# Kernel optimization log

Hardware: AMD Instinct MI355X
Metric: run time of the kernel (lower is better)

The kernel has to match this reference:

```python
import jax, jax.numpy as jnp
import numpy as np

# Dimensions
B2, T, C = 400, 120, 128          # x: ((B*V), T, C)
V = 25                            # num_point (skeleton joints)
NH_A = 3                          # adjacency heads (A.shape[0])
HEADS, DH = 8, 64                 # attention heads, dim_head
INNER = HEADS * DH                # 512
QKV_C = INNER * 3                 # 1536 = GCN out_channels
EPS = 1e-5                        # torch BatchNorm2d default eps


def setup_inputs() -> dict:
    key = jax.random.key(0)
    ks = jax.random.split(key, 12)
    z = lambda *s: jnp.zeros(s, jnp.float32)
    o = lambda *s: jnp.ones(s, jnp.float32)
    return {
        "x": jax.random.normal(ks[0], (B2, T, C), jnp.float32),
        # GCN shared topology (num_head, V, V)
        "A": jax.random.normal(ks[1], (NH_A, V, V), jnp.float32) * 0.2,
        # per-head 1x1 conv weights/biases (stacked)
        "conv_w": jax.random.normal(ks[2], (NH_A, QKV_C, C), jnp.float32) * 0.02,
        "conv_b": jax.random.normal(ks[3], (NH_A, QKV_C), jnp.float32) * 0.01,
        # main BatchNorm2d (eval mode, running stats)
        "bn_gamma": jax.random.uniform(ks[4], (QKV_C,), jnp.float32, 0.5, 1.5),
        "bn_beta": z(QKV_C),
        "bn_mean": z(QKV_C),
        "bn_var": o(QKV_C),
        # down path: 1x1 conv + BatchNorm2d (in_c != out_c)
        "down_w": jax.random.normal(ks[5], (QKV_C, C), jnp.float32) * 0.02,
        "down_b": z(QKV_C),
        "dbn_gamma": jax.random.uniform(ks[6], (QKV_C,), jnp.float32, 0.5, 1.5),
        "dbn_beta": z(QKV_C),
        "dbn_mean": z(QKV_C),
        "dbn_var": o(QKV_C),
        # to_out Linear(inner_dim -> dim)
        "out_w": jax.random.normal(ks[7], (C, INNER), jnp.float32) * 0.02,
        "out_b": z(C),
    }


def _bn_eval(y, gamma, beta, mean, var):
    # y: (b, o, t, v); BN over channel axis 1, eval mode
    inv = gamma / jnp.sqrt(var + EPS)
    return y * inv[None, :, None, None] + (beta - mean * inv)[None, :, None, None]


def reference(x, A, conv_w, conv_b, bn_gamma, bn_beta, bn_mean, bn_var,
              down_w, down_b, dbn_gamma, dbn_beta, dbn_mean, dbn_var,
              out_w, out_b):
    B = B2 // V
    # '(b v) t c -> b c t v'
    x4 = x.reshape(B, V, T, C).transpose(0, 3, 2, 1)  # (b, c, t, v)

    # ---- GCN projection: sum_h Conv1x1_h(A_h @ x) ----
    z = jnp.einsum('hvu,bctu->bhctv', A, x4)                    # (b,h,c,t,v)
    y = jnp.einsum('hoc,bhctv->botv', conv_w, z)                # (b,O,t,v)
    y = y + conv_b.sum(0)[None, :, None, None]
    y = _bn_eval(y, bn_gamma, bn_beta, bn_mean, bn_var)

    d = jnp.einsum('oc,bctv->botv', down_w, x4) + down_b[None, :, None, None]
    d = _bn_eval(d, dbn_gamma, dbn_beta, dbn_mean, dbn_var)

    y = jax.nn.relu(y + d)                                      # (b,O,t,v)

    # ---- attention over time per (batch*joint) row ----
    qkv = y.transpose(0, 3, 2, 1).reshape(B2, T, QKV_C)         # '(b v) t c'
    q, k, v = jnp.split(qkv, 3, axis=-1)
    split_heads = lambda t: t.reshape(B2, T, HEADS, DH).transpose(0, 2, 1, 3)
    q, k, v = split_heads(q), split_heads(k), split_heads(v)

    dots = jnp.einsum('bhid,bhjd->bhij', q, k) * (DH ** -0.5)
    mask = jnp.tril(jnp.ones((T, T), bool))                     # causal mask
    dots = jnp.where(mask[None, None], dots, -jnp.inf)
    attn = jax.nn.softmax(dots, axis=-1)                        # (B2,H,T,T)

    o = jnp.einsum('bhij,bhjd->bhid', attn, v)
    o = o.transpose(0, 2, 1, 3).reshape(B2, T, INNER)
    out = o @ out_w.T + out_b                                   # (B2,T,C)
    return out, attn
```

## Files before the change

kernel.cpp:

```cpp
#include <hip/hip_runtime.h>


typedef __bf16 bf16;
typedef __bf16 bf16x8 __attribute__((ext_vector_type(8)));
typedef __bf16 bf16x4 __attribute__((ext_vector_type(4)));
typedef float  f32x4  __attribute__((ext_vector_type(4)));
typedef __attribute__((address_space(1))) const void* gptr1;
typedef __attribute__((address_space(3))) void*       lptr3;

#define GLL16(g, l) __builtin_amdgcn_global_load_lds((gptr1)(g), (lptr3)(l), 16, 0, 0)
#define MFMA16(a, b, c) __builtin_amdgcn_mfma_f32_16x16x32_bf16(a, b, c, 0, 0, 0)

__global__ __launch_bounds__(256) void build_weights(
    const float* __restrict__ conv_w, const float* __restrict__ conv_b,
    const float* __restrict__ g1, const float* __restrict__ be1,
    const float* __restrict__ mu1, const float* __restrict__ va1,
    const float* __restrict__ down_w, const float* __restrict__ down_b,
    const float* __restrict__ g2, const float* __restrict__ be2,
    const float* __restrict__ mu2, const float* __restrict__ va2,
    const float* __restrict__ out_w,
    bf16* __restrict__ wcat, bf16* __restrict__ wout, float* __restrict__ bias)
{
    int idx = blockIdx.x * 256 + threadIdx.x;
    if (idx < 1536 * 512) {
        int o = idx >> 9, k = idx & 511;
        float s, w;
        if (k < 384) {
            int h = k >> 7, c = k & 127;
            s = g1[o] * rsqrtf(va1[o] + 1e-5f);
            w = conv_w[(h * 1536 + o) * 128 + c];
        } else {
            s = g2[o] * rsqrtf(va2[o] + 1e-5f);
            w = down_w[o * 128 + (k - 384)];
        }
        wcat[idx] = (bf16)(w * s);
    }
    int i2 = idx - 1536 * 512;
    if (i2 >= 0 && i2 < 128 * 512) wout[i2] = (bf16)out_w[i2];
    int i3 = idx - (1536 * 512 + 128 * 512);
    if (i3 >= 0 && i3 < 1536) {
        int o = i3;
        float s1 = g1[o] * rsqrtf(va1[o] + 1e-5f);
        float s2 = g2[o] * rsqrtf(va2[o] + 1e-5f);
        float cb = conv_b[o] + conv_b[1536 + o] + conv_b[2 * 1536 + o];
        bias[o] = cb * s1 + be1[o] - mu1[o] * s1
                + down_b[o] * s2 + be2[o] - mu2[o] * s2;
    }
}

__global__ __launch_bounds__(256) void transform(
    const float* __restrict__ x, const float* __restrict__ A,
    bf16* __restrict__ zt)
{
    __shared__ float xs[25][128];
    const int tid = threadIdx.x;
    const int bt = blockIdx.x;
    const int b = bt / 120, t = bt - b * 120;
    for (int i = tid; i < 25 * 128; i += 256) {
        int u = i >> 7, c = i & 127;
        xs[u][c] = x[((size_t)(b * 25 + u) * 120 + t) * 128 + c];
    }
    __syncthreads();
    const int c = tid & 127, g = tid >> 7;
    float xr[25];
    #pragma unroll
    for (int u = 0; u < 25; u++) xr[u] = xs[u][c];
    for (int idx = g; idx < 75; idx += 2) {
        int h = idx / 25, v = idx - h * 25;
        const float* Ap = A + (h * 25 + v) * 25;
        float acc = 0.f;
        #pragma unroll
        for (int u = 0; u < 25; u++) acc += Ap[u] * xr[u];
        zt[((size_t)(b * 25 + v) * 120 + t) * 512 + h * 128 + c] = (bf16)acc;
    }
    for (int v = g; v < 25; v += 2)
        zt[((size_t)(b * 25 + v) * 120 + t) * 512 + 384 + c] = (bf16)xs[v][c];
}

__global__ __launch_bounds__(256) void gemm_qkv(
    const bf16* __restrict__ wcat, const bf16* __restrict__ zt,
    const float* __restrict__ bias,
    bf16* __restrict__ qg, bf16* __restrict__ kg, bf16* __restrict__ vtg)
{
    __shared__ __align__(16) char smem[49152];
    const int tid = threadIdx.x, lane = tid & 63, wv = tid >> 6;
    const int wrow = wv >> 1, wcol = wv & 1;
    const int NB = 4500, q8 = NB >> 3, r8 = NB & 7;
    const int xcd = blockIdx.x & 7, sidx = blockIdx.x >> 3;
    const int vid = (xcd < r8 ? xcd * (q8 + 1) : r8 * (q8 + 1) + (xcd - r8) * q8) + sidx;
    const int mt = vid % 12, nt = vid / 12;
    const int colb = lane & 15, rg = lane >> 4;

    f32x4 zz = {0.f, 0.f, 0.f, 0.f};
    f32x4 acc[4][4];
    #pragma unroll
    for (int i = 0; i < 4; i++)
        #pragma unroll
        for (int j = 0; j < 4; j++) acc[i][j] = zz;

    const char* gA = (const char*)wcat + (size_t)mt * 128 * 1024;
    const char* gB = (const char*)zt + (size_t)nt * 128 * 1024;
    const int srow = lane >> 2;
    const int skb = (((lane & 3) ^ ((lane >> 3) & 3)) * 16);
    const int rgs = rg ^ ((colb >> 1) & 3);
    const int aoff0 = (wrow * 64 + colb) * 64 + rgs * 16;
    const int boff0 = (wcol * 64 + colb) * 64 + rgs * 16;

    #define STAGE_QKV(kt, b) do {                                              \
        char* As_ = smem + (b) * 16384; char* Bs_ = As_ + 8192;                \
        _Pragma("unroll")                                                      \
        for (int j = 0; j < 2; j++) {                                          \
            int ck = wv * 2 + j;  int row = ck * 16 + srow;                    \
            GLL16(gA + (size_t)row * 1024 + (kt) * 64 + skb, As_ + ck * 1024); \
            GLL16(gB + (size_t)row * 1024 + (kt) * 64 + skb, Bs_ + ck * 1024); \
        } } while (0)

    STAGE_QKV(0, 0);
    STAGE_QKV(1, 1);
    asm volatile("s_waitcnt vmcnt(4)" ::: "memory");
    __builtin_amdgcn_s_barrier();
    for (int kt = 0; kt < 16; kt++) {
        const char* As = smem + (kt % 3) * 16384;
        const char* Bs = As + 8192;
        bf16x8 af[4], bfr[4];
        #pragma unroll
        for (int m = 0; m < 4; m++)
            af[m] = *(const bf16x8*)(As + aoff0 + m * 1024);
        #pragma unroll
        for (int n = 0; n < 4; n++)
            bfr[n] = *(const bf16x8*)(Bs + boff0 + n * 1024);
        int kn = kt + 2;
        STAGE_QKV(kn < 16 ? kn : 15, kn % 3);
        __builtin_amdgcn_s_setprio(1);
        #pragma unroll
        for (int m = 0; m < 4; m++)
            #pragma unroll
            for (int n = 0; n < 4; n++)
                acc[m][n] = MFMA16(af[m], bfr[n], acc[m][n]);
        __builtin_amdgcn_s_setprio(0);
        asm volatile("s_waitcnt vmcnt(4)" ::: "memory");
        __builtin_amdgcn_s_barrier();
    }
    __builtin_amdgcn_sched_barrier(0);

    const int mtb = mt * 128, ntb = nt * 128;
    const int which = mtb >> 9;

    if (which < 2) {
        bf16* Lt = (bf16*)smem;
        const float qs = (which == 0) ? 0.125f : 1.0f;
        #pragma unroll
        for (int m = 0; m < 4; m++) {
            int o0 = wrow * 64 + m * 16 + rg * 4;
            float b0 = bias[mtb + o0 + 0], b1 = bias[mtb + o0 + 1];
            float b2 = bias[mtb + o0 + 2], b3 = bias[mtb + o0 + 3];
            #pragma unroll
            for (int nn = 0; nn < 4; nn++) {
                int n_ = wcol * 64 + nn * 16 + colb;
                bf16x4 pk;
                pk[0] = (bf16)(fmaxf(acc[m][nn][0] + b0, 0.f) * qs);
                pk[1] = (bf16)(fmaxf(acc[m][nn][1] + b1, 0.f) * qs);
                pk[2] = (bf16)(fmaxf(acc[m][nn][2] + b2, 0.f) * qs);
                pk[3] = (bf16)(fmaxf(acc[m][nn][3] + b3, 0.f) * qs);
                *(bf16x4*)((char*)Lt + n_ * 256 + ((o0 * 2) ^ ((n_ & 7) << 4))) = pk;
            }
        }
        __syncthreads();
        bf16* dst = (which == 0) ? qg : kg;
        #pragma unroll
        for (int i = 0; i < 8; i++) {
            int ch = i * 256 + tid;
            int n_ = ch >> 4, c16 = ch & 15;
            int ng = ntb + n_;
            int grp = ng / 120, t = ng - grp * 120;
            int o = mtb + c16 * 8;
            int hd = (o >> 6) & 7, dd0 = o & 63;
            bf16x8 vv = *(const bf16x8*)((const char*)Lt + n_ * 256 +
                                         ((c16 * 16) ^ ((n_ & 7) << 4)));
            *(bf16x8*)(dst + ((size_t)(grp * 8 + hd) * 120 + t) * 64 + dd0) = vv;
        }
    } else {
        #pragma unroll
        for (int m = 0; m < 4; m++) {
            #pragma unroll
            for (int reg = 0; reg < 4; reg++) {
                int o = mtb + wrow * 64 + m * 16 + rg * 4 + reg;
                float bo = bias[o];
                int hd = (o >> 6) & 7, dd = o & 63;
                #pragma unroll
                for (int nn = 0; nn < 4; nn++) {
                    int n = ntb + wcol * 64 + nn * 16 + colb;
                    int grp = n / 120, t = n - grp * 120;
                    float val = fmaxf(acc[m][nn][reg] + bo, 0.f);
                    vtg[((size_t)(grp * 8 + hd) * 64 + dd) * 128 + t] = (bf16)val;
                }
            }
        }
    }
    #undef STAGE_QKV
}

__global__ __launch_bounds__(256) void attn_k(
    const bf16* __restrict__ qg, const bf16* __restrict__ kg,
    const bf16* __restrict__ vtg, float* __restrict__ attn_out,
    bf16* __restrict__ og)
{
    __shared__ __align__(16) char sm[49152];
    char* Vt = sm;
    char* Ks = sm + 16384;
    char* Ps = sm + 16384;
    const int tid = threadIdx.x, lane = tid & 63, wv = tid >> 6;
    const int bh = blockIdx.x;
    const int colb = lane & 15, rg = lane >> 4;

    const char* ksrc = (const char*)kg + (size_t)bh * 15360;
    const char* vsrc = (const char*)vtg + (size_t)bh * 16384;
    #pragma unroll
    for (int is = 0; is < 4; is++) {
        int cb = is * 256 + wv * 64;
        if (cb < 960) {
            int bb = (cb + lane) * 16;
            int row = bb >> 7;
            int gsrc = (bb & ~127) | ((bb & 127) ^ ((row & 7) << 4));
            GLL16(ksrc + gsrc, Ks + cb * 16);
        }
    }
    const char* qsrc = (const char*)qg + (size_t)bh * 15360;
    bf16x8 qf[2][2];
    #pragma unroll
    for (int kk = 0; kk < 2; kk++)
        #pragma unroll
        for (int m = 0; m < 2; m++) {
            int row = wv * 32 + m * 16 + colb;
            qf[kk][m] = *(const bf16x8*)(qsrc + (size_t)row * 128 + rg * 16 + kk * 64);
        }
    #pragma unroll
    for (int is = 0; is < 4; is++) {
        int cb = is * 256 + wv * 64;
        int bb = (cb + lane) * 16;
        int row = bb >> 8;
        int gsrc = (bb & ~255) | ((bb & 255) ^ ((row & 7) << 4));
        GLL16(vsrc + gsrc, Vt + cb * 16);
    }
    asm volatile("s_waitcnt vmcnt(4)" ::: "memory");
    __builtin_amdgcn_s_barrier();
    if (tid < 64) {
        f32x4 z = {0.f, 0.f, 0.f, 0.f};
        int r = 120 + (tid >> 3), off = (tid & 7) * 16;
        *(f32x4*)(Ks + r * 128 + off) = z;
    }
    asm volatile("s_waitcnt lgkmcnt(0)" ::: "memory");
    __builtin_amdgcn_s_barrier();

    f32x4 accs[2][8];
    #pragma unroll
    for (int m = 0; m < 2; m++)
        #pragma unroll
        for (int ct = 0; ct < 8; ct++) accs[m][ct] = (f32x4){0.f, 0.f, 0.f, 0.f};
    #pragma unroll
    for (int kk = 0; kk < 2; kk++) {
        #pragma unroll
        for (int ct = 0; ct < 8; ct++) {
            int rk = ct * 16 + colb;
            int byo = rk * 128 + ((rg * 16 + kk * 64) ^ ((rk & 7) << 4));
            bf16x8 bk = *(const bf16x8*)(Ks + byo);
            accs[0][ct] = MFMA16(qf[kk][0], bk, accs[0][ct]);
            accs[1][ct] = MFMA16(qf[kk][1], bk, accs[1][ct]);
        }
    }
    asm volatile("s_waitcnt vmcnt(0)" ::: "memory");
    __builtin_amdgcn_s_barrier();
    if (tid >= 64 && tid < 128) {
        int d = tid - 64;
        f32x4 z = {0.f, 0.f, 0.f, 0.f};
        *(f32x4*)(Vt + d * 256 + (240 ^ ((d & 7) << 4))) = z;
    }

    const int rqb = wv * 32;
    #pragma unroll
    for (int m = 0; m < 2; m++) {
        #pragma unroll
        for (int reg = 0; reg < 4; reg++) {
            int t_q = rqb + m * 16 + rg * 4 + reg;
            float s[8], mx = -1e30f;
            #pragma unroll
            for (int ct = 0; ct < 8; ct++) {
                int col = ct * 16 + colb;
                bool valid = (col <= t_q) && (col < 120);
                s[ct] = valid ? accs[m][ct][reg] : -1e30f;
                mx = fmaxf(mx, s[ct]);
            }
            #pragma unroll
            for (int d = 1; d < 16; d <<= 1) mx = fmaxf(mx, __shfl_xor(mx, d, 64));
            float p[8], sum = 0.f;
            #pragma unroll
            for (int ct = 0; ct < 8; ct++) {
                p[ct] = (s[ct] > -1e29f) ? __expf(s[ct] - mx) : 0.f;
                sum += p[ct];
            }
            #pragma unroll
            for (int d = 1; d < 16; d <<= 1) sum += __shfl_xor(sum, d, 64);
            float inv = 1.f / sum;
            #pragma unroll
            for (int ct = 0; ct < 8; ct++) {
                int col = ct * 16 + colb;
                int byo = t_q * 256 + ((col * 2) ^ ((t_q & 7) << 4));
                *(bf16*)(Ps + byo) = (bf16)(p[ct] * inv);
            }
        }
    }
    asm volatile("s_waitcnt lgkmcnt(0)" ::: "memory");
    __builtin_amdgcn_s_barrier();

    f32x4 acco[2][4];
    #pragma unroll
    for (int m = 0; m < 2; m++)
        #pragma unroll
        for (int dt = 0; dt < 4; dt++) acco[m][dt] = (f32x4){0.f, 0.f, 0.f, 0.f};
    for (int kk = 0; kk <= wv; kk++) {
        bf16x8 ap[2];
        #pragma unroll
        for (int m = 0; m < 2; m++) {
            int row = rqb + m * 16 + colb;
            int byo = row * 256 + ((rg * 16 + kk * 64) ^ ((row & 7) << 4));
            ap[m] = *(const bf16x8*)(Ps + byo);
        }
        #pragma unroll
        for (int dt = 0; dt < 4; dt++) {
            int rd = dt * 16 + colb;
            int byo = rd * 256 + ((rg * 16 + kk * 64) ^ ((rd & 7) << 4));
            bf16x8 bv = *(const bf16x8*)(Vt + byo);
            acco[0][dt] = MFMA16(ap[0], bv, acco[0][dt]);
            acco[1][dt] = MFMA16(ap[1], bv, acco[1][dt]);
        }
    }

    {
        float* attn_base = attn_out + (size_t)bh * 14400;
        #pragma unroll
        for (int i = 0; i < 15; i++) {
            int chunk = i * 256 + tid;
            if (chunk < 3600) {
                int r = chunk / 30, c4 = chunk - r * 30;
                int byo = r * 256 + ((c4 * 8) ^ ((r & 7) << 4));
                bf16x4 pv4 = *(const bf16x4*)(Ps + byo);
                f32x4 o4 = { (float)pv4[0], (float)pv4[1],
                             (float)pv4[2], (float)pv4[3] };
                *(f32x4*)(attn_base + chunk * 4) = o4;
            }
        }
    }

    const int b2 = bh >> 3, h = bh & 7;
    #pragma unroll
    for (int m = 0; m < 2; m++)
        #pragma unroll
        for (int dt = 0; dt < 4; dt++)
            #pragma unroll
            for (int reg = 0; reg < 4; reg++) {
                int t = rqb + m * 16 + rg * 4 + reg;
                if (t < 120) {
                    int dfull = h * 64 + dt * 16 + colb;
                    og[((size_t)b2 * 120 + t) * 512 + dfull] = (bf16)acco[m][dt][reg];
                }
            }
}

__global__ __launch_bounds__(256) void gemm_out_k(
    const bf16* __restrict__ og, const bf16* __restrict__ wout,
    const float* __restrict__ outb, float* __restrict__ out)
{
    __shared__ __align__(16) char smem[49152];
    const int tid = threadIdx.x, lane = tid & 63, wv = tid >> 6;
    const int wrow = wv >> 1, wcol = wv & 1;
    const int nt = blockIdx.x;
    const int colb = lane & 15, rg = lane >> 4;

    f32x4 zz = {0.f, 0.f, 0.f, 0.f};
    f32x4 acc[4][4];
    #pragma unroll
    for (int i = 0; i < 4; i++)
        #pragma unroll
        for (int j = 0; j < 4; j++) acc[i][j] = zz;

    const char* gA = (const char*)og + (size_t)nt * 128 * 1024;
    const char* gB = (const char*)wout;
    const int srow = lane >> 2;
    const int skb = (((lane & 3) ^ ((lane >> 3) & 3)) * 16);
    const int rgs = rg ^ ((colb >> 1) & 3);
    const int aoff0 = (wrow * 64 + colb) * 64 + rgs * 16;
    const int boff0 = (wcol * 64 + colb) * 64 + rgs * 16;

    #define STAGE_OUT(kt, b) do {                                              \
        char* As_ = smem + (b) * 16384; char* Bs_ = As_ + 8192;                \
        _Pragma("unroll")                                                      \
        for (int j = 0; j < 2; j++) {                                          \
            int ck = wv * 2 + j;  int row = ck * 16 + srow;                    \
            GLL16(gA + (size_t)row * 1024 + (kt) * 64 + skb, As_ + ck * 1024); \
            GLL16(gB + (size_t)row * 1024 + (kt) * 64 + skb, Bs_ + ck * 1024); \
        } } while (0)

    STAGE_OUT(0, 0);
    STAGE_OUT(1, 1);
    asm volatile("s_waitcnt vmcnt(4)" ::: "memory");
    __builtin_amdgcn_s_barrier();
    for (int kt = 0; kt < 16; kt++) {
        const char* As = smem + (kt % 3) * 16384;
        const char* Bs = As + 8192;
        bf16x8 af[4], bfr[4];
        #pragma unroll
        for (int m = 0; m < 4; m++)
            af[m] = *(const bf16x8*)(As + aoff0 + m * 1024);
        #pragma unroll
        for (int n = 0; n < 4; n++)
            bfr[n] = *(const bf16x8*)(Bs + boff0 + n * 1024);
        int kn = kt + 2;
        STAGE_OUT(kn < 16 ? kn : 15, kn % 3);
        __builtin_amdgcn_s_setprio(1);
        #pragma unroll
        for (int m = 0; m < 4; m++)
            #pragma unroll
            for (int n = 0; n < 4; n++)
                acc[m][n] = MFMA16(af[m], bfr[n], acc[m][n]);
        __builtin_amdgcn_s_setprio(0);
        asm volatile("s_waitcnt vmcnt(4)" ::: "memory");
        __builtin_amdgcn_s_barrier();
    }
    __builtin_amdgcn_sched_barrier(0);

    const int rbase = nt * 128 + wrow * 64;
    #pragma unroll
    for (int m = 0; m < 4; m++)
        #pragma unroll
        for (int reg = 0; reg < 4; reg++) {
            int r = rbase + m * 16 + rg * 4 + reg;
            #pragma unroll
            for (int nn = 0; nn < 4; nn++) {
                int c = wcol * 64 + nn * 16 + colb;
                out[(size_t)r * 128 + c] = acc[m][nn][reg] + outb[c];
            }
        }
    #undef STAGE_OUT
}

extern "C" void kernel_launch(void* const* d_in, const int* in_sizes, int n_in,
                              void* d_out, int out_size, void* d_ws, size_t ws_size,
                              hipStream_t stream)
{
    (void)in_sizes; (void)n_in; (void)out_size; (void)ws_size;
    const float* x      = (const float*)d_in[0];
    const float* A      = (const float*)d_in[1];
    const float* conv_w = (const float*)d_in[2];
    const float* conv_b = (const float*)d_in[3];
    const float* bn_g   = (const float*)d_in[4];
    const float* bn_b   = (const float*)d_in[5];
    const float* bn_m   = (const float*)d_in[6];
    const float* bn_v   = (const float*)d_in[7];
    const float* dw     = (const float*)d_in[8];
    const float* db     = (const float*)d_in[9];
    const float* dg     = (const float*)d_in[10];
    const float* dbb    = (const float*)d_in[11];
    const float* dm     = (const float*)d_in[12];
    const float* dvv    = (const float*)d_in[13];
    const float* out_w  = (const float*)d_in[14];
    const float* out_b  = (const float*)d_in[15];

    char* ws = (char*)d_ws;
    const size_t OFF_WCAT = 0;
    const size_t OFF_WOUT = 1572864;
    const size_t OFF_BIAS = 1703936;
    const size_t OFF_ZT   = 1710080;
    const size_t OFF_Q    = 50862080;
    const size_t OFF_K    = 100014080;
    const size_t OFF_VT   = 149166080;
    const size_t OFF_O    = OFF_ZT;

    bf16*  wcat = (bf16*)(ws + OFF_WCAT);
    bf16*  wout = (bf16*)(ws + OFF_WOUT);
    float* bias = (float*)(ws + OFF_BIAS);
    bf16*  zt   = (bf16*)(ws + OFF_ZT);
    bf16*  qg   = (bf16*)(ws + OFF_Q);
    bf16*  kg   = (bf16*)(ws + OFF_K);
    bf16*  vtg  = (bf16*)(ws + OFF_VT);
    bf16*  og   = (bf16*)(ws + OFF_O);
    float* outp = (float*)d_out;
    float* attn = outp + 6144000;

    build_weights<<<3334, 256, 0, stream>>>(conv_w, conv_b, bn_g, bn_b, bn_m, bn_v,
                                            dw, db, dg, dbb, dm, dvv, out_w,
                                            wcat, wout, bias);
    transform<<<1920, 256, 0, stream>>>(x, A, zt);
    gemm_qkv<<<4500, 256, 0, stream>>>(wcat, zt, bias, qg, kg, vtg);
    attn_k<<<3200, 256, 0, stream>>>(qg, kg, vtg, attn, og);
    gemm_out_k<<<375, 256, 0, stream>>>(og, wout, out_b, outp);
}
```

Before: 273.0 us.

## Switch GEMM mainloops to BK=64 double-buffered tiles with XOR swizzle

```diff
diff --git a/kernel.cpp b/kernel.cpp
--- a/kernel.cpp
+++ b/kernel.cpp
@@ -82,7 +82,7 @@
     const float* __restrict__ bias,
     bf16* __restrict__ qg, bf16* __restrict__ kg, bf16* __restrict__ vtg)
 {
-    __shared__ __align__(16) char smem[49152];
+    __shared__ __align__(16) char smem[65536];
     const int tid = threadIdx.x, lane = tid & 63, wv = tid >> 6;
     const int wrow = wv >> 1, wcol = wv & 1;
     const int NB = 4500, q8 = NB >> 3, r8 = NB & 7;
@@ -91,54 +91,60 @@
     const int mt = vid % 12, nt = vid / 12;
     const int colb = lane & 15, rg = lane >> 4;
 
-    f32x4 zz = {0.f, 0.f, 0.f, 0.f};
     f32x4 acc[4][4];
     #pragma unroll
     for (int i = 0; i < 4; i++)
         #pragma unroll
-        for (int j = 0; j < 4; j++) acc[i][j] = zz;
+        for (int j = 0; j < 4; j++) acc[i][j] = (f32x4){0.f, 0.f, 0.f, 0.f};
 
     const char* gA = (const char*)wcat + (size_t)mt * 128 * 1024;
     const char* gB = (const char*)zt + (size_t)nt * 128 * 1024;
-    const int srow = lane >> 2;
-    const int skb = (((lane & 3) ^ ((lane >> 3) & 3)) * 16);
-    const int rgs = rg ^ ((colb >> 1) & 3);
-    const int aoff0 = (wrow * 64 + colb) * 64 + rgs * 16;
-    const int boff0 = (wcol * 64 + colb) * 64 + rgs * 16;
-
-    #define STAGE_QKV(kt, b) do {                                              \
-        char* As_ = smem + (b) * 16384; char* Bs_ = As_ + 8192;                \
-        _Pragma("unroll")                                                      \
-        for (int j = 0; j < 2; j++) {                                          \
-            int ck = wv * 2 + j;  int row = ck * 16 + srow;                    \
-            GLL16(gA + (size_t)row * 1024 + (kt) * 64 + skb, As_ + ck * 1024); \
-            GLL16(gB + (size_t)row * 1024 + (kt) * 64 + skb, Bs_ + ck * 1024); \
+
+    int aoff[4][2], boff[4][2];
+    #pragma unroll
+    for (int m = 0; m < 4; m++)
+        #pragma unroll
+        for (int kk = 0; kk < 2; kk++) {
+            int swz = (rg * 16 + kk * 64) ^ ((colb & 7) << 4);
+            aoff[m][kk] = (wrow * 64 + m * 16 + colb) * 128 + swz;
+            boff[m][kk] = (wcol * 64 + m * 16 + colb) * 128 + swz;
+        }
+
+    #define STG(kt, bsel) do {                                                  \
+        char* As_ = smem + (bsel) * 32768; char* Bs_ = As_ + 16384;             \
+        _Pragma("unroll")                                                       \
+        for (int j = 0; j < 4; j++) {                                           \
+            int c = j * 256 + tid;                                              \
+            int r = c >> 3, sl = (c & 7) ^ (r & 7);                             \
+            GLL16(gA + (size_t)r * 1024 + (kt) * 128 + sl * 16, As_ + c * 16);  \
+            GLL16(gB + (size_t)r * 1024 + (kt) * 128 + sl * 16, Bs_ + c * 16);  \
         } } while (0)
 
-    STAGE_QKV(0, 0);
-    STAGE_QKV(1, 1);
-    asm volatile("s_waitcnt vmcnt(4)" ::: "memory");
+    STG(0, 0);
+    asm volatile("s_waitcnt vmcnt(0)" ::: "memory");
     __builtin_amdgcn_s_barrier();
-    for (int kt = 0; kt < 16; kt++) {
-        const char* As = smem + (kt % 3) * 16384;
-        const char* Bs = As + 8192;
-        bf16x8 af[4], bfr[4];
+    for (int p = 0; p < 8; p++) {
+        const char* As = smem + (p & 1) * 32768;
+        const char* Bs = As + 16384;
+        if (p < 7) STG(p + 1, (p + 1) & 1);
+        bf16x8 af[4][2], bfr[4][2];
         #pragma unroll
         for (int m = 0; m < 4; m++)
-            af[m] = *(const bf16x8*)(As + aoff0 + m * 1024);
-        #pragma unroll
-        for (int n = 0; n < 4; n++)
-            bfr[n] = *(const bf16x8*)(Bs + boff0 + n * 1024);
-        int kn = kt + 2;
-        STAGE_QKV(kn < 16 ? kn : 15, kn % 3);
+            #pragma unroll
+            for (int kk = 0; kk < 2; kk++) {
+                af[m][kk]  = *(const bf16x8*)(As + aoff[m][kk]);
+                bfr[m][kk] = *(const bf16x8*)(Bs + boff[m][kk]);
+            }
         __builtin_amdgcn_s_setprio(1);
         #pragma unroll
         for (int m = 0; m < 4; m++)
             #pragma unroll
             for (int n = 0; n < 4; n++)
-                acc[m][n] = MFMA16(af[m], bfr[n], acc[m][n]);
+                #pragma unroll
+                for (int kk = 0; kk < 2; kk++)
+                    acc[m][n] = MFMA16(af[m][kk], bfr[n][kk], acc[m][n]);
         __builtin_amdgcn_s_setprio(0);
-        asm volatile("s_waitcnt vmcnt(4)" ::: "memory");
+        asm volatile("s_waitcnt vmcnt(0)" ::: "memory");
         __builtin_amdgcn_s_barrier();
     }
     __builtin_amdgcn_sched_barrier(0);
@@ -197,7 +203,7 @@
             }
         }
     }
-    #undef STAGE_QKV
+    #undef STG
 }
 
 __global__ __launch_bounds__(256) void attn_k(
@@ -370,60 +376,66 @@
     const bf16* __restrict__ og, const bf16* __restrict__ wout,
     const float* __restrict__ outb, float* __restrict__ out)
 {
-    __shared__ __align__(16) char smem[49152];
+    __shared__ __align__(16) char smem[65536];
     const int tid = threadIdx.x, lane = tid & 63, wv = tid >> 6;
     const int wrow = wv >> 1, wcol = wv & 1;
     const int nt = blockIdx.x;
     const int colb = lane & 15, rg = lane >> 4;
 
-    f32x4 zz = {0.f, 0.f, 0.f, 0.f};
     f32x4 acc[4][4];
     #pragma unroll
     for (int i = 0; i < 4; i++)
         #pragma unroll
-        for (int j = 0; j < 4; j++) acc[i][j] = zz;
+        for (int j = 0; j < 4; j++) acc[i][j] = (f32x4){0.f, 0.f, 0.f, 0.f};
 
     const char* gA = (const char*)og + (size_t)nt * 128 * 1024;
     const char* gB = (const char*)wout;
-    const int srow = lane >> 2;
-    const int skb = (((lane & 3) ^ ((lane >> 3) & 3)) * 16);
-    const int rgs = rg ^ ((colb >> 1) & 3);
-    const int aoff0 = (wrow * 64 + colb) * 64 + rgs * 16;
-    const int boff0 = (wcol * 64 + colb) * 64 + rgs * 16;
-
-    #define STAGE_OUT(kt, b) do {                                              \
-        char* As_ = smem + (b) * 16384; char* Bs_ = As_ + 8192;                \
-        _Pragma("unroll")                                                      \
-        for (int j = 0; j < 2; j++) {                                          \
-            int ck = wv * 2 + j;  int row = ck * 16 + srow;                    \
-            GLL16(gA + (size_t)row * 1024 + (kt) * 64 + skb, As_ + ck * 1024); \
-            GLL16(gB + (size_t)row * 1024 + (kt) * 64 + skb, Bs_ + ck * 1024); \
+
+    int aoff[4][2], boff[4][2];
+    #pragma unroll
+    for (int m = 0; m < 4; m++)
+        #pragma unroll
+        for (int kk = 0; kk < 2; kk++) {
+            int swz = (rg * 16 + kk * 64) ^ ((colb & 7) << 4);
+            aoff[m][kk] = (wrow * 64 + m * 16 + colb) * 128 + swz;
+            boff[m][kk] = (wcol * 64 + m * 16 + colb) * 128 + swz;
+        }
+
+    #define STG_O(kt, bsel) do {                                                \
+        char* As_ = smem + (bsel) * 32768; char* Bs_ = As_ + 16384;             \
+        _Pragma("unroll")                                                       \
+        for (int j = 0; j < 4; j++) {                                           \
+            int c = j * 256 + tid;                                              \
+            int r = c >> 3, sl = (c & 7) ^ (r & 7);                             \
+            GLL16(gA + (size_t)r * 1024 + (kt) * 128 + sl * 16, As_ + c * 16);  \
+            GLL16(gB + (size_t)r * 1024 + (kt) * 128 + sl * 16, Bs_ + c * 16);  \
         } } while (0)
 
-    STAGE_OUT(0, 0);
-    STAGE_OUT(1, 1);
-    asm volatile("s_waitcnt vmcnt(4)" ::: "memory");
+    STG_O(0, 0);
+    asm volatile("s_waitcnt vmcnt(0)" ::: "memory");
     __builtin_amdgcn_s_barrier();
-    for (int kt = 0; kt < 16; kt++) {
-        const char* As = smem + (kt % 3) * 16384;
-        const char* Bs = As + 8192;
-        bf16x8 af[4], bfr[4];
+    for (int p = 0; p < 8; p++) {
+        const char* As = smem + (p & 1) * 32768;
+        const char* Bs = As + 16384;
+        if (p < 7) STG_O(p + 1, (p + 1) & 1);
+        bf16x8 af[4][2], bfr[4][2];
         #pragma unroll
         for (int m = 0; m < 4; m++)
-            af[m] = *(const bf16x8*)(As + aoff0 + m * 1024);
-        #pragma unroll
-        for (int n = 0; n < 4; n++)
-            bfr[n] = *(const bf16x8*)(Bs + boff0 + n * 1024);
-        int kn = kt + 2;
-        STAGE_OUT(kn < 16 ? kn : 15, kn % 3);
+            #pragma unroll
+            for (int kk = 0; kk < 2; kk++) {
+                af[m][kk]  = *(const bf16x8*)(As + aoff[m][kk]);
+                bfr[m][kk] = *(const bf16x8*)(Bs + boff[m][kk]);
+            }
         __builtin_amdgcn_s_setprio(1);
         #pragma unroll
         for (int m = 0; m < 4; m++)
             #pragma unroll
             for (int n = 0; n < 4; n++)
-                acc[m][n] = MFMA16(af[m], bfr[n], acc[m][n]);
+                #pragma unroll
+                for (int kk = 0; kk < 2; kk++)
+                    acc[m][n] = MFMA16(af[m][kk], bfr[n][kk], acc[m][n]);
         __builtin_amdgcn_s_setprio(0);
-        asm volatile("s_waitcnt vmcnt(4)" ::: "memory");
+        asm volatile("s_waitcnt vmcnt(0)" ::: "memory");
         __builtin_amdgcn_s_barrier();
     }
     __builtin_amdgcn_sched_barrier(0);
@@ -440,7 +452,7 @@
                 out[(size_t)r * 128 + c] = acc[m][nn][reg] + outb[c];
             }
         }
-    #undef STAGE_OUT
+    #undef STG_O
 }
 
 extern "C" void kernel_launch(void* const* d_in, const int* in_sizes, int n_in,
```

Result: faster. 262.9 us, median of 3 (-3.7%).
